# Kernel optimization log

Hardware: AMD Instinct MI355X
Metric: run time of the kernel (lower is better)

## Reference

```python
import jax, jax.numpy as jnp
import numpy as np

L_IN, L_K = 1, 1            # degree ranges (0..L)
C_IN, K_CH, H = 16, 8, 4    # in_channels, k_channels (per head), num_heads
C_OUT = H * K_CH            # 32
E, N_NODES, EMB = 32768, 4096, 64
M_IN, M_K = (L_IN + 1) ** 2, (L_K + 1) ** 2


def _so2_pairs(L_in, L_out):
    # enumerate SO(2)-equivariant weight blocks: for each order m, all (l_in, l_out)
    # pairs with l >= m; m=0 uses 1 matrix, m>0 uses 2 (real/imag parts).
    pairs, w = [], 0
    for m in range(min(L_in, L_out) + 1):
        for l_in in range(m, L_in + 1):
            for l_out in range(m, L_out + 1):
                pairs.append((m, l_in, l_out, w))
                w += 1 if m == 0 else 2
    return pairs, w

_PAIRS, NUM_W = _so2_pairs(L_IN, L_K)  # NUM_W = 6 for L_in=L_k=1


def so2_linear(x, W, L_in, L_out):
    # x: [E, (L_in+1)^2, Cin]; W: [NUM_W, Cin, Cout] (shared) or [E, NUM_W, Cin, Cout] (per-edge)
    per_edge = (W.ndim == 4)
    Cout = W.shape[-1]
    out = jnp.zeros((x.shape[0], (L_out + 1) ** 2, Cout), x.dtype)

    def mat(xs, w):
        return jnp.einsum('ec,eco->eo', xs, W[:, w]) if per_edge else xs @ W[w]

    pairs, _ = _so2_pairs(L_in, L_out)
    for m, l_in, l_out, w in pairs:
        i_in, i_out = l_in * (l_in + 1), l_out * (l_out + 1)  # flat index of (l, m=0)
        if m == 0:
            out = out.at[:, i_out].add(mat(x[:, i_in], w))
        else:
            xp, xn = x[:, i_in + m], x[:, i_in - m]
            out = out.at[:, i_out + m].add(mat(xp, w) - mat(xn, w + 1))
            out = out.at[:, i_out - m].add(mat(xp, w + 1) + mat(xn, w))
    return out


def segment_softmax(z, index, num_segments):
    # PyG-style softmax over ragged neighborhoods (max is detached, as in PyG)
    zmax = jax.lax.stop_gradient(jax.ops.segment_max(z, index, num_segments=num_segments))
    e = jnp.exp(z - zmax[index])
    denom = jax.ops.segment_sum(e, index, num_segments=num_segments)
    return e / denom[index]


def setup_inputs() -> dict:
    key = jax.random.key(0)
    ks = jax.random.split(key, 6)
    x_q = jax.random.normal(ks[0], (E, M_IN, C_IN), jnp.float32)
    x_k = jax.random.normal(ks[1], (E, M_IN, C_IN), jnp.float32)
    edge_emb = jax.random.normal(ks[2], (E, EMB), jnp.float32)
    index = jnp.sort(jax.random.randint(ks[3], (E,), 0, N_NODES))
    W_q = jax.random.normal(ks[4], (NUM_W, C_IN, C_OUT), jnp.float32) / np.sqrt(C_IN)
    W_p = jax.random.normal(ks[5], (EMB, NUM_W * C_IN * C_OUT), jnp.float32) / np.sqrt(EMB)
    return {"x_q": x_q, "x_k": x_k, "edge_emb": edge_emb, "index": index,
            "W_q": W_q, "W_p": W_p, "num_nodes": N_NODES}


def reference(x_q, x_k, edge_emb, index, W_q, W_p, num_nodes):
    # q_ij = W_Q x_i ; static SO2 weights
    q = so2_linear(x_q, W_q, L_IN, L_K).reshape(-1, M_K, H, K_CH)
    # k_ij = W_K(||r_ij||) x_j ; per-edge dynamic SO2 weights from edge embedding
    W_k = (edge_emb @ W_p).reshape(-1, NUM_W, C_IN, C_OUT)
    k = so2_linear(x_k, W_k, L_IN, L_K).reshape(-1, M_K, H, K_CH)
    scale = (K_CH // H) ** (-0.5)  # faithful to original: (k_channels // num_heads)**-0.5
    z = (q * k).sum((-1, -3)) * scale  # [E, H]
    return segment_softmax(z, index, num_nodes)
```

## Files before the change

### kernel.cpp

```cpp
#include <hip/hip_runtime.h>
#include <math.h>

#define E_TOTAL 32768
#define NUM_NODES 4096
#define SCALE 0.70710678118654752f

typedef __attribute__((ext_vector_type(8))) short bfrag;
typedef __attribute__((ext_vector_type(16))) float facc;

__device__ inline unsigned short f2bf(float f) {
  unsigned int u = __float_as_uint(f);
  unsigned int r = (u + 0x7FFFu + ((u >> 16) & 1u)) >> 16;
  return (unsigned short)r;
}
__device__ inline float bf2f(unsigned short s) {
  return __uint_as_float(((unsigned int)s) << 16);
}
__device__ inline void cvt8(const float* v, bfrag& hi, bfrag& lo) {
#pragma unroll
  for (int i = 0; i < 8; ++i) {
    unsigned short h = f2bf(v[i]);
    hi[i] = (short)h;
    lo[i] = (short)f2bf(v[i] - bf2f(h));
  }
}

__global__ __launch_bounds__(256) void prep_kernel(
    const float* __restrict__ Wp, const float* __restrict__ Wq,
    const int* __restrict__ index,
    unsigned short* __restrict__ fragWp, unsigned short* __restrict__ fragWq,
    int* __restrict__ offs)
{
  const int b = blockIdx.x, t = threadIdx.x;
  if (b < 96) {
    __shared__ unsigned short lds[4096];
    const int c = b / 6, w = b - c * 6;
    const int colbase = w * 512 + c * 32;
    const int cl = t & 31, dg = t >> 5;
#pragma unroll
    for (int i = 0; i < 8; ++i) {
      const int d = dg * 8 + i;
      const float v = Wp[(size_t)d * 3072 + colbase + cl];
      const unsigned short hi = f2bf(v);
      const unsigned short lo = f2bf(v - bf2f(hi));
      const int ks = d >> 4;
      const int lane = ((d >> 3) & 1) * 32 + cl;
      const int j = d & 7;
      lds[(ks * 2 + 0) * 512 + lane * 8 + j] = hi;
      lds[(ks * 2 + 1) * 512 + lane * 8 + j] = lo;
    }
    __syncthreads();
    unsigned short* dst = fragWp + (size_t)b * 4096;
    ((uint4*)dst)[t] = ((const uint4*)lds)[t];
    ((uint4*)dst)[t + 256] = ((const uint4*)lds)[t + 256];
  } else if (b < 103) {
    const int slot = b - 96;
    const int w = (slot == 6) ? 5 : slot;
    const float sgn = (slot == 6) ? -1.f : 1.f;
    for (int tt = t; tt < 512; tt += 256) {
      const int lane = tt >> 3, j = tt & 7;
      const int o = lane & 31, c = (lane >> 5) * 8 + j;
      const float v = sgn * Wq[(size_t)(w * 16 + c) * 32 + o];
      const unsigned short hi = f2bf(v);
      const unsigned short lo = f2bf(v - bf2f(hi));
      fragWq[slot * 1024 + lane * 8 + j] = hi;
      fragWq[slot * 1024 + 512 + lane * 8 + j] = lo;
    }
  } else {
    const int tg = (b - 103) * 256 + t;
    if (tg >= E_TOTAL) return;
    const int cur = index[tg];
    const int prev = (tg == 0) ? -1 : index[tg - 1];
    for (int n = prev + 1; n <= cur; ++n) offs[n] = tg;
    if (tg == E_TOTAL - 1)
      for (int n = cur + 1; n <= NUM_NODES; ++n) offs[n] = E_TOTAL;
  }
}

__global__ __launch_bounds__(256, 2) void main_kernel(
    const float* __restrict__ x_q, const float* __restrict__ x_k,
    const float* __restrict__ emb,
    const unsigned short* __restrict__ fragWp,
    const unsigned short* __restrict__ fragWq,
    float* __restrict__ z)
{
  __shared__ float xk_t[64][65];
  __shared__ float zred[4][32][4];

  const int t = threadIdx.x;
  const int lane = t & 63, wv = t >> 6;
  const int pr = wv & 1;
  const int col = lane & 31, half = lane >> 5;
  const int eb = blockIdx.x * 64;
  const int el = (wv >> 1) * 32 + col;
  const int e = eb + el;

  {
    const int er = t >> 2, dq = (t & 3) * 16;
    const float* src = x_k + (size_t)(eb + er) * 64 + dq;
#pragma unroll
    for (int i = 0; i < 4; ++i) {
      float4 v = *(const float4*)(src + i * 4);
      xk_t[dq + i * 4 + 0][er] = v.x;
      xk_t[dq + i * 4 + 1][er] = v.y;
      xk_t[dq + i * 4 + 2][er] = v.z;
      xk_t[dq + i * 4 + 3][er] = v.w;
    }
  }

  bfrag ebh[4], ebl[4];
#pragma unroll
  for (int ks = 0; ks < 4; ++ks) {
    float tmp[8];
    *(float4*)&tmp[0] = *(const float4*)(emb + (size_t)e * 64 + ks * 16 + half * 8);
    *(float4*)&tmp[4] = *(const float4*)(emb + (size_t)e * 64 + ks * 16 + half * 8 + 4);
    cvt8(tmp, ebh[ks], ebl[ks]);
  }

  facc ka0 = {0}, ka1 = {0}, ka2 = {0}, ka3 = {0};

  const unsigned short* fbase = fragWp + pr * 4096 + lane * 8;

  bfrag curh[4], curl[4], nxth[4], nxtl[4];
#pragma unroll
  for (int ks = 0; ks < 4; ++ks) {
    *(uint4*)&curh[ks] = *(const uint4*)(fbase + ks * 1024);
    *(uint4*)&curl[ks] = *(const uint4*)(fbase + ks * 1024 + 512);
  }

  __syncthreads();

  float xkc0 = 0.f, xkc1 = 0.f, xkc2 = 0.f, xkc3 = 0.f;

#pragma unroll 6
  for (int it = 0; it < 48; ++it) {
    const int j = it % 3;
    {
      const int itn = (it < 47) ? it + 1 : 47;
      const unsigned short* gp = fbase + (size_t)itn * 8192;
#pragma unroll
      for (int ks = 0; ks < 4; ++ks) {
        *(uint4*)&nxth[ks] = *(const uint4*)(gp + ks * 1024);
        *(uint4*)&nxtl[ks] = *(const uint4*)(gp + ks * 1024 + 512);
      }
    }
    if (j == 0) {
      const int c16 = it / 3;
      xkc0 = xk_t[c16][el];
      xkc1 = xk_t[16 + c16][el];
      xkc2 = xk_t[32 + c16][el];
      xkc3 = xk_t[48 + c16][el];
    }
    facc cc0 = {0.f}, cc1 = {0.f}, cc2 = {0.f};
#pragma unroll
    for (int ks = 0; ks < 4; ++ks) {
      cc0 = __builtin_amdgcn_mfma_f32_32x32x16_bf16(curh[ks], ebh[ks], cc0, 0, 0, 0);
      cc1 = __builtin_amdgcn_mfma_f32_32x32x16_bf16(curh[ks], ebl[ks], cc1, 0, 0, 0);
      cc2 = __builtin_amdgcn_mfma_f32_32x32x16_bf16(curl[ks], ebh[ks], cc2, 0, 0, 0);
    }
    if (j < 2) {
      const float xv = (j == 0) ? xkc0 : xkc2;
      if (pr == 0) {
#pragma unroll
        for (int r = 0; r < 16; ++r)
          ka0[r] = fmaf(xv, cc0[r] + cc1[r] + cc2[r], ka0[r]);
      } else {
#pragma unroll
        for (int r = 0; r < 16; ++r)
          ka2[r] = fmaf(xv, cc0[r] + cc1[r] + cc2[r], ka2[r]);
      }
    } else {
      if (pr == 0) {
#pragma unroll
        for (int r = 0; r < 16; ++r) {
          const float s = cc0[r] + cc1[r] + cc2[r];
          ka1[r] = fmaf(xkc1, s, ka1[r]);
          ka3[r] = fmaf(xkc3, s, ka3[r]);
        }
      } else {
#pragma unroll
        for (int r = 0; r < 16; ++r) {
          const float s = cc0[r] + cc1[r] + cc2[r];
          ka1[r] = fmaf(xkc3, s, ka1[r]);
          ka3[r] = fmaf(-xkc1, s, ka3[r]);
        }
      }
    }
#pragma unroll
    for (int ks = 0; ks < 4; ++ks) { curh[ks] = nxth[ks]; curl[ks] = nxtl[ks]; }
  }

  bfrag xqh[4], xql[4];
#pragma unroll
  for (int a = 0; a < 4; ++a) {
    float tmp[8];
    *(float4*)&tmp[0] = *(const float4*)(x_q + (size_t)e * 64 + a * 16 + half * 8);
    *(float4*)&tmp[4] = *(const float4*)(x_q + (size_t)e * 64 + a * 16 + half * 8 + 4);
    cvt8(tmp, xqh[a], xql[a]);
  }
  float zp0 = 0.f, zp1 = 0.f, zp2 = 0.f, zp3 = 0.f;
  const int QA1[4] = {0, 1, 0, 3}, QS1[4] = {0, 4, 1, 4};
  const int QA2[4] = {2, 3, 2, 1}, QS2[4] = {2, 5, 3, 6};
#pragma unroll
  for (int m = 0; m < 4; ++m) {
    facc qa = {0.f};
#pragma unroll
    for (int tm = 0; tm < 2; ++tm) {
      const int a = tm ? QA2[m] : QA1[m];
      const int sl = tm ? QS2[m] : QS1[m];
      bfrag wh, wl;
      *(uint4*)&wh = *(const uint4*)(fragWq + sl * 1024 + lane * 8);
      *(uint4*)&wl = *(const uint4*)(fragWq + sl * 1024 + 512 + lane * 8);
      qa = __builtin_amdgcn_mfma_f32_32x32x16_bf16(wh, xqh[a], qa, 0, 0, 0);
      qa = __builtin_amdgcn_mfma_f32_32x32x16_bf16(wh, xql[a], qa, 0, 0, 0);
      qa = __builtin_amdgcn_mfma_f32_32x32x16_bf16(wl, xqh[a], qa, 0, 0, 0);
    }
    const facc& km = (m == 0) ? ka0 : (m == 1) ? ka1 : (m == 2) ? ka2 : ka3;
#pragma unroll
    for (int r = 0; r < 16; ++r) {
      const float v = qa[r] * km[r];
      if (r < 4) zp0 += v;
      else if (r < 8) zp1 += v;
      else if (r < 12) zp2 += v;
      else zp3 += v;
    }
  }
  zp0 += __shfl_xor(zp0, 32);
  zp1 += __shfl_xor(zp1, 32);
  zp2 += __shfl_xor(zp2, 32);
  zp3 += __shfl_xor(zp3, 32);
  if (half == 0) {
    float4 v = {zp0, zp1, zp2, zp3};
    *(float4*)&zred[wv][col][0] = v;
  }
  __syncthreads();
  if (pr == 0 && half == 0) {
    float4 a = *(const float4*)&zred[wv][col][0];
    float4 b = *(const float4*)&zred[wv ^ 1][col][0];
    float4 o = {(a.x + b.x) * SCALE, (a.y + b.y) * SCALE,
                (a.z + b.z) * SCALE, (a.w + b.w) * SCALE};
    *(float4*)&z[(size_t)e * 4] = o;
  }
}

__global__ __launch_bounds__(256) void softmax_kernel(
    const float* __restrict__ z, const int* __restrict__ offs,
    float* __restrict__ out)
{
  const int node = blockIdx.x * 4 + (threadIdx.x >> 6);
  const int lane = threadIdx.x & 63;
  const int start = offs[node], end = offs[node + 1];
  if (start >= end) return;
  const int h = lane & 3, eo = lane >> 2;
  float m = -INFINITY;
  for (int e = start + eo; e < end; e += 16) m = fmaxf(m, z[(size_t)e * 4 + h]);
#pragma unroll
  for (int s = 4; s < 64; s <<= 1) m = fmaxf(m, __shfl_xor(m, s));
  float sum = 0.f;
  for (int e = start + eo; e < end; e += 16) sum += __expf(z[(size_t)e * 4 + h] - m);
#pragma unroll
  for (int s = 4; s < 64; s <<= 1) sum += __shfl_xor(sum, s);
  const float inv = 1.f / sum;
  for (int e = start + eo; e < end; e += 16)
    out[(size_t)e * 4 + h] = __expf(z[(size_t)e * 4 + h] - m) * inv;
}

extern "C" void kernel_launch(void* const* d_in, const int* in_sizes, int n_in,
                              void* d_out, int out_size, void* d_ws, size_t ws_size,
                              hipStream_t stream) {
  const float* x_q = (const float*)d_in[0];
  const float* x_k = (const float*)d_in[1];
  const float* emb = (const float*)d_in[2];
  const int* index = (const int*)d_in[3];
  const float* W_q = (const float*)d_in[4];
  const float* W_p = (const float*)d_in[5];
  float* out = (float*)d_out;

  char* ws = (char*)d_ws;
  float* z = (float*)ws;
  int* offs = (int*)(ws + 524288);
  unsigned short* fragWp = (unsigned short*)(ws + 524288 + 32768);
  unsigned short* fragWq = (unsigned short*)(ws + 524288 + 32768 + 786432);

  prep_kernel<<<231, 256, 0, stream>>>(W_p, W_q, index, fragWp, fragWq, offs);
  main_kernel<<<512, 256, 0, stream>>>(x_q, x_k, emb, fragWp, fragWq, z);
  softmax_kernel<<<1024, 256, 0, stream>>>(z, offs, out);
}
```

Before: 119.9 us.

## Split per-edge weight contraction across four waves per 32-edge block

Each block now handles 32 edges instead of 64, and the four waves split the 48 weight-fragment iterations four ways (24 fragment loads each, over a quarter of the input channels) instead of two waves per edge group splitting by parity. Partial k-accumulations are reduced across all four waves through shared memory. The grid doubles to 1024 blocks for more parallelism, and two of the three bf16 split-precision MFMA accumulators are merged into one. The cost is that each block reloads the weight fragments for only half as many edges, so weight traffic per edge roughly doubles, and the final reduction step is larger.

```diff
diff --git a/kernel.cpp b/kernel.cpp
--- a/kernel.cpp
+++ b/kernel.cpp
@@ -84,22 +84,20 @@
     const unsigned short* __restrict__ fragWq,
     float* __restrict__ z)
 {
-  __shared__ float xk_t[64][65];
+  __shared__ float xk_t[64][33];
   __shared__ float zred[4][32][4];
 
   const int t = threadIdx.x;
   const int lane = t & 63, wv = t >> 6;
-  const int pr = wv & 1;
   const int col = lane & 31, half = lane >> 5;
-  const int eb = blockIdx.x * 64;
-  const int el = (wv >> 1) * 32 + col;
-  const int e = eb + el;
+  const int eb = blockIdx.x * 32;
+  const int e = eb + col;
 
   {
-    const int er = t >> 2, dq = (t & 3) * 16;
+    const int er = t >> 3, dq = (t & 7) * 8;
     const float* src = x_k + (size_t)(eb + er) * 64 + dq;
 #pragma unroll
-    for (int i = 0; i < 4; ++i) {
+    for (int i = 0; i < 2; ++i) {
       float4 v = *(const float4*)(src + i * 4);
       xk_t[dq + i * 4 + 0][er] = v.x;
       xk_t[dq + i * 4 + 1][er] = v.y;
@@ -119,7 +117,7 @@
 
   facc ka0 = {0}, ka1 = {0}, ka2 = {0}, ka3 = {0};
 
-  const unsigned short* fbase = fragWp + pr * 4096 + lane * 8;
+  const unsigned short* fbase = fragWp + (size_t)wv * 24 * 4096 + lane * 8;
 
   bfrag curh[4], curl[4], nxth[4], nxtl[4];
 #pragma unroll
@@ -133,11 +131,11 @@
   float xkc0 = 0.f, xkc1 = 0.f, xkc2 = 0.f, xkc3 = 0.f;
 
 #pragma unroll 6
-  for (int it = 0; it < 48; ++it) {
-    const int j = it % 3;
+  for (int it = 0; it < 24; ++it) {
+    const int j = it % 6;
     {
-      const int itn = (it < 47) ? it + 1 : 47;
-      const unsigned short* gp = fbase + (size_t)itn * 8192;
+      const int itn = (it < 23) ? it + 1 : 23;
+      const unsigned short* gp = fbase + (size_t)itn * 4096;
 #pragma unroll
       for (int ks = 0; ks < 4; ++ks) {
         *(uint4*)&nxth[ks] = *(const uint4*)(gp + ks * 1024);
@@ -145,45 +143,38 @@
       }
     }
     if (j == 0) {
-      const int c16 = it / 3;
-      xkc0 = xk_t[c16][el];
-      xkc1 = xk_t[16 + c16][el];
-      xkc2 = xk_t[32 + c16][el];
-      xkc3 = xk_t[48 + c16][el];
-    }
-    facc cc0 = {0.f}, cc1 = {0.f}, cc2 = {0.f};
+      const int c16 = (wv << 2) + it / 6;
+      xkc0 = xk_t[c16][col];
+      xkc1 = xk_t[16 + c16][col];
+      xkc2 = xk_t[32 + c16][col];
+      xkc3 = xk_t[48 + c16][col];
+    }
+    facc cc0 = {0.f}, cc12 = {0.f};
 #pragma unroll
     for (int ks = 0; ks < 4; ++ks) {
-      cc0 = __builtin_amdgcn_mfma_f32_32x32x16_bf16(curh[ks], ebh[ks], cc0, 0, 0, 0);
-      cc1 = __builtin_amdgcn_mfma_f32_32x32x16_bf16(curh[ks], ebl[ks], cc1, 0, 0, 0);
-      cc2 = __builtin_amdgcn_mfma_f32_32x32x16_bf16(curl[ks], ebh[ks], cc2, 0, 0, 0);
-    }
-    if (j < 2) {
-      const float xv = (j == 0) ? xkc0 : xkc2;
-      if (pr == 0) {
-#pragma unroll
-        for (int r = 0; r < 16; ++r)
-          ka0[r] = fmaf(xv, cc0[r] + cc1[r] + cc2[r], ka0[r]);
-      } else {
-#pragma unroll
-        for (int r = 0; r < 16; ++r)
-          ka2[r] = fmaf(xv, cc0[r] + cc1[r] + cc2[r], ka2[r]);
+      cc0  = __builtin_amdgcn_mfma_f32_32x32x16_bf16(curh[ks], ebh[ks], cc0, 0, 0, 0);
+      cc12 = __builtin_amdgcn_mfma_f32_32x32x16_bf16(curh[ks], ebl[ks], cc12, 0, 0, 0);
+      cc12 = __builtin_amdgcn_mfma_f32_32x32x16_bf16(curl[ks], ebh[ks], cc12, 0, 0, 0);
+    }
+    if (j < 4) {
+      const float xv = (j & 2) ? xkc2 : xkc0;
+      facc& kd = (j & 1) ? ka2 : ka0;
+#pragma unroll
+      for (int r = 0; r < 16; ++r)
+        kd[r] = fmaf(xv, cc0[r] + cc12[r], kd[r]);
+    } else if (j == 4) {
+#pragma unroll
+      for (int r = 0; r < 16; ++r) {
+        const float s = cc0[r] + cc12[r];
+        ka1[r] = fmaf(xkc1, s, ka1[r]);
+        ka3[r] = fmaf(xkc3, s, ka3[r]);
       }
     } else {
-      if (pr == 0) {
-#pragma unroll
-        for (int r = 0; r < 16; ++r) {
-          const float s = cc0[r] + cc1[r] + cc2[r];
-          ka1[r] = fmaf(xkc1, s, ka1[r]);
-          ka3[r] = fmaf(xkc3, s, ka3[r]);
-        }
-      } else {
-#pragma unroll
-        for (int r = 0; r < 16; ++r) {
-          const float s = cc0[r] + cc1[r] + cc2[r];
-          ka1[r] = fmaf(xkc3, s, ka1[r]);
-          ka3[r] = fmaf(-xkc1, s, ka3[r]);
-        }
+#pragma unroll
+      for (int r = 0; r < 16; ++r) {
+        const float s = cc0[r] + cc12[r];
+        ka1[r] = fmaf(xkc3, s, ka1[r]);
+        ka3[r] = fmaf(-xkc1, s, ka3[r]);
       }
     }
 #pragma unroll
@@ -234,11 +225,15 @@
     *(float4*)&zred[wv][col][0] = v;
   }
   __syncthreads();
-  if (pr == 0 && half == 0) {
-    float4 a = *(const float4*)&zred[wv][col][0];
-    float4 b = *(const float4*)&zred[wv ^ 1][col][0];
-    float4 o = {(a.x + b.x) * SCALE, (a.y + b.y) * SCALE,
-                (a.z + b.z) * SCALE, (a.w + b.w) * SCALE};
+  if (wv == 0 && half == 0) {
+    float4 a0 = *(const float4*)&zred[0][col][0];
+    float4 a1 = *(const float4*)&zred[1][col][0];
+    float4 a2 = *(const float4*)&zred[2][col][0];
+    float4 a3 = *(const float4*)&zred[3][col][0];
+    float4 o = {(a0.x + a1.x + a2.x + a3.x) * SCALE,
+                (a0.y + a1.y + a2.y + a3.y) * SCALE,
+                (a0.z + a1.z + a2.z + a3.z) * SCALE,
+                (a0.w + a1.w + a2.w + a3.w) * SCALE};
     *(float4*)&z[(size_t)e * 4] = o;
   }
 }
@@ -283,6 +278,6 @@
   unsigned short* fragWq = (unsigned short*)(ws + 524288 + 32768 + 786432);
 
   prep_kernel<<<231, 256, 0, stream>>>(W_p, W_q, index, fragWp, fragWq, offs);
-  main_kernel<<<512, 256, 0, stream>>>(x_q, x_k, emb, fragWp, fragWq, z);
+  main_kernel<<<1024, 256, 0, stream>>>(x_q, x_k, emb, fragWp, fragWq, z);
   softmax_kernel<<<1024, 256, 0, stream>>>(z, offs, out);
 }
```

Result: slower. 126.6 us (+5.6%).

## Give each wave all output columns for its own edges, removing cross-wave reduction

Applied to the files above, without the earlier changes.

Each wave previously handled half of the output-channel pairs (pr) for 32 edges, and the two halves were combined through shared memory. Now each block covers 128 edges and each wave computes every output column for its 32 edges, walking all 96 weight-fragment steps. This drops the zred shared-memory reduction and doubles reuse of the edge-embedding fragments. In exchange the grid is halved to 256 blocks, occupancy is capped at one block per SM, and a __syncthreads is added every 24 iterations, so latency hiding may suffer.

```diff
diff --git a/kernel.cpp b/kernel.cpp
--- a/kernel.cpp
+++ b/kernel.cpp
@@ -77,34 +77,32 @@
   }
 }
 
-__global__ __launch_bounds__(256, 2) void main_kernel(
+__global__ __launch_bounds__(256, 1) void main_kernel(
     const float* __restrict__ x_q, const float* __restrict__ x_k,
     const float* __restrict__ emb,
     const unsigned short* __restrict__ fragWp,
     const unsigned short* __restrict__ fragWq,
     float* __restrict__ z)
 {
-  __shared__ float xk_t[64][65];
-  __shared__ float zred[4][32][4];
+  __shared__ float xk_t[64][129];
 
   const int t = threadIdx.x;
   const int lane = t & 63, wv = t >> 6;
-  const int pr = wv & 1;
   const int col = lane & 31, half = lane >> 5;
-  const int eb = blockIdx.x * 64;
-  const int el = (wv >> 1) * 32 + col;
+  const int eb = blockIdx.x * 128;
+  const int el = wv * 32 + col;
   const int e = eb + el;
 
   {
-    const int er = t >> 2, dq = (t & 3) * 16;
-    const float* src = x_k + (size_t)(eb + er) * 64 + dq;
-#pragma unroll
-    for (int i = 0; i < 4; ++i) {
+    const int er = t & 127, dh = (t >> 7) * 32;
+    const float* src = x_k + (size_t)(eb + er) * 64 + dh;
+#pragma unroll
+    for (int i = 0; i < 8; ++i) {
       float4 v = *(const float4*)(src + i * 4);
-      xk_t[dq + i * 4 + 0][er] = v.x;
-      xk_t[dq + i * 4 + 1][er] = v.y;
-      xk_t[dq + i * 4 + 2][er] = v.z;
-      xk_t[dq + i * 4 + 3][er] = v.w;
+      xk_t[dh + i * 4 + 0][er] = v.x;
+      xk_t[dh + i * 4 + 1][er] = v.y;
+      xk_t[dh + i * 4 + 2][er] = v.z;
+      xk_t[dh + i * 4 + 3][er] = v.w;
     }
   }
 
@@ -119,7 +117,7 @@
 
   facc ka0 = {0}, ka1 = {0}, ka2 = {0}, ka3 = {0};
 
-  const unsigned short* fbase = fragWp + pr * 4096 + lane * 8;
+  const unsigned short* fbase = fragWp + lane * 8;
 
   bfrag curh[4], curl[4], nxth[4], nxtl[4];
 #pragma unroll
@@ -132,45 +130,41 @@
 
   float xkc0 = 0.f, xkc1 = 0.f, xkc2 = 0.f, xkc3 = 0.f;
 
+  for (int ot = 0; ot < 4; ++ot) {
 #pragma unroll 6
-  for (int it = 0; it < 48; ++it) {
-    const int j = it % 3;
-    {
-      const int itn = (it < 47) ? it + 1 : 47;
-      const unsigned short* gp = fbase + (size_t)itn * 8192;
+    for (int ii = 0; ii < 24; ++ii) {
+      const int it = ot * 24 + ii;
+      const int j = ii % 6;
+      {
+        const int itn = (it < 95) ? it + 1 : 95;
+        const unsigned short* gp = fbase + (size_t)itn * 4096;
+#pragma unroll
+        for (int ks = 0; ks < 4; ++ks) {
+          *(uint4*)&nxth[ks] = *(const uint4*)(gp + ks * 1024);
+          *(uint4*)&nxtl[ks] = *(const uint4*)(gp + ks * 1024 + 512);
+        }
+      }
+      if (j == 0) {
+        const int c16 = it / 6;
+        xkc0 = xk_t[c16][el];
+        xkc1 = xk_t[16 + c16][el];
+        xkc2 = xk_t[32 + c16][el];
+        xkc3 = xk_t[48 + c16][el];
+      }
+      facc cc0 = {0.f}, cc1 = {0.f}, cc2 = {0.f};
 #pragma unroll
       for (int ks = 0; ks < 4; ++ks) {
-        *(uint4*)&nxth[ks] = *(const uint4*)(gp + ks * 1024);
-        *(uint4*)&nxtl[ks] = *(const uint4*)(gp + ks * 1024 + 512);
-      }
-    }
-    if (j == 0) {
-      const int c16 = it / 3;
-      xkc0 = xk_t[c16][el];
-      xkc1 = xk_t[16 + c16][el];
-      xkc2 = xk_t[32 + c16][el];
-      xkc3 = xk_t[48 + c16][el];
-    }
-    facc cc0 = {0.f}, cc1 = {0.f}, cc2 = {0.f};
-#pragma unroll
-    for (int ks = 0; ks < 4; ++ks) {
-      cc0 = __builtin_amdgcn_mfma_f32_32x32x16_bf16(curh[ks], ebh[ks], cc0, 0, 0, 0);
-      cc1 = __builtin_amdgcn_mfma_f32_32x32x16_bf16(curh[ks], ebl[ks], cc1, 0, 0, 0);
-      cc2 = __builtin_amdgcn_mfma_f32_32x32x16_bf16(curl[ks], ebh[ks], cc2, 0, 0, 0);
-    }
-    if (j < 2) {
-      const float xv = (j == 0) ? xkc0 : xkc2;
-      if (pr == 0) {
+        cc0 = __builtin_amdgcn_mfma_f32_32x32x16_bf16(curh[ks], ebh[ks], cc0, 0, 0, 0);
+        cc1 = __builtin_amdgcn_mfma_f32_32x32x16_bf16(curh[ks], ebl[ks], cc1, 0, 0, 0);
+        cc2 = __builtin_amdgcn_mfma_f32_32x32x16_bf16(curl[ks], ebh[ks], cc2, 0, 0, 0);
+      }
+      if (j < 4) {
+        const float xv = (j & 2) ? xkc2 : xkc0;
+        facc& kd = (j & 1) ? ka2 : ka0;
 #pragma unroll
         for (int r = 0; r < 16; ++r)
-          ka0[r] = fmaf(xv, cc0[r] + cc1[r] + cc2[r], ka0[r]);
-      } else {
-#pragma unroll
-        for (int r = 0; r < 16; ++r)
-          ka2[r] = fmaf(xv, cc0[r] + cc1[r] + cc2[r], ka2[r]);
-      }
-    } else {
-      if (pr == 0) {
+          kd[r] = fmaf(xv, cc0[r] + cc1[r] + cc2[r], kd[r]);
+      } else if (j == 4) {
 #pragma unroll
         for (int r = 0; r < 16; ++r) {
           const float s = cc0[r] + cc1[r] + cc2[r];
@@ -185,9 +179,10 @@
           ka3[r] = fmaf(-xkc1, s, ka3[r]);
         }
       }
-    }
-#pragma unroll
-    for (int ks = 0; ks < 4; ++ks) { curh[ks] = nxth[ks]; curl[ks] = nxtl[ks]; }
+#pragma unroll
+      for (int ks = 0; ks < 4; ++ks) { curh[ks] = nxth[ks]; curl[ks] = nxtl[ks]; }
+    }
+    __syncthreads();
   }
 
   bfrag xqh[4], xql[4];
@@ -230,16 +225,8 @@
   zp2 += __shfl_xor(zp2, 32);
   zp3 += __shfl_xor(zp3, 32);
   if (half == 0) {
-    float4 v = {zp0, zp1, zp2, zp3};
-    *(float4*)&zred[wv][col][0] = v;
-  }
-  __syncthreads();
-  if (pr == 0 && half == 0) {
-    float4 a = *(const float4*)&zred[wv][col][0];
-    float4 b = *(const float4*)&zred[wv ^ 1][col][0];
-    float4 o = {(a.x + b.x) * SCALE, (a.y + b.y) * SCALE,
-                (a.z + b.z) * SCALE, (a.w + b.w) * SCALE};
-    *(float4*)&z[(size_t)e * 4] = o;
+    float4 v = {zp0 * SCALE, zp1 * SCALE, zp2 * SCALE, zp3 * SCALE};
+    *(float4*)&z[(size_t)e * 4] = v;
   }
 }
 
@@ -283,6 +270,6 @@
   unsigned short* fragWq = (unsigned short*)(ws + 524288 + 32768 + 786432);
 
   prep_kernel<<<231, 256, 0, stream>>>(W_p, W_q, index, fragWp, fragWq, offs);
-  main_kernel<<<512, 256, 0, stream>>>(x_q, x_k, emb, fragWp, fragWq, z);
+  main_kernel<<<256, 256, 0, stream>>>(x_q, x_k, emb, fragWp, fragWq, z);
   softmax_kernel<<<1024, 256, 0, stream>>>(z, offs, out);
 }
```

Measured after the change: 124.7 us. 4.1% more time.
